# Kernel optimization log

Hardware: AMD Instinct MI355X
Metric: run time of the kernel (lower is better)

## Reference

```python
import jax, jax.numpy as jnp
import numpy as np

NU, NI = 100000, 50000      # global embedding table sizes
U, I = 50000, 20000         # nodes in this subgraph
E = 400000                  # edges per direction
HID, H = 512, 8
D = HID // H                # out_feats per head = 64
NEG_SLOPE = 0.2


def setup_inputs() -> dict:
    key = jax.random.key(0)
    ks = jax.random.split(key, 16)
    s = 1.0 / np.sqrt(HID)
    a = 1.0 / np.sqrt(D)
    return {
        'u_gid': jax.random.randint(ks[0], (U,), 0, NU),
        'i_gid': jax.random.randint(ks[1], (I,), 0, NI),
        'src_u': jax.random.randint(ks[2], (E,), 0, U),
        'dst_i': jax.random.randint(ks[3], (E,), 0, I),
        'user_emb': jax.random.normal(ks[4], (NU, HID), jnp.float32) * 0.02,
        'item_emb': jax.random.normal(ks[5], (NI, HID), jnp.float32) * 0.02,
        # 'interact' (user -> item) GATConv params
        'W_ui': jax.random.normal(ks[6], (HID, HID), jnp.float32) * s,
        'al_ui': jax.random.normal(ks[7], (H, D), jnp.float32) * a,
        'ar_ui': jax.random.normal(ks[8], (H, D), jnp.float32) * a,
        'b_ui': jnp.zeros((HID,), jnp.float32),
        # 'interact_rev' (item -> user) GATConv params
        'W_iu': jax.random.normal(ks[9], (HID, HID), jnp.float32) * s,
        'al_iu': jax.random.normal(ks[10], (H, D), jnp.float32) * a,
        'ar_iu': jax.random.normal(ks[11], (H, D), jnp.float32) * a,
        'b_iu': jnp.zeros((HID,), jnp.float32),
    }


def gat_conv(h_src, h_dst, src, dst, W, attn_l, attn_r, bias, n_dst):
    """DGL GATConv (eval mode, allow_zero_in_degree): [n_dst, H, D]."""
    fs = (h_src @ W).reshape(-1, H, D)            # [Ns,H,D]
    fd = (h_dst @ W).reshape(-1, H, D)            # [Nd,H,D]
    el = jnp.sum(fs * attn_l, axis=-1)            # [Ns,H]
    er = jnp.sum(fd * attn_r, axis=-1)            # [Nd,H]
    e = jax.nn.leaky_relu(el[src] + er[dst], NEG_SLOPE)   # [E,H]
    # segment softmax over incoming edges of each destination
    emax = jax.ops.segment_max(e, dst, num_segments=n_dst)[dst]
    ex = jnp.exp(e - emax)                        # [E,H]
    denom = jax.ops.segment_sum(ex, dst, num_segments=n_dst)[dst]
    alpha = ex / denom                            # [E,H]
    msg = fs[src] * alpha[:, :, None]             # [E,H,D]
    out = jax.ops.segment_sum(msg, dst, num_segments=n_dst)  # zero for isolated dst
    return out + bias.reshape(1, H, D)


def reference(u_gid, i_gid, src_u, dst_i, user_emb, item_emb,
              W_ui, al_ui, ar_ui, b_ui, W_iu, al_iu, ar_iu, b_iu):
    h_u0 = user_emb[u_gid]                        # [U,HID]
    h_i0 = item_emb[i_gid]                        # [I,HID]
    # 'interact': user -> item
    h_item = gat_conv(h_u0, h_i0, src_u, dst_i, W_ui, al_ui, ar_ui, b_ui, I)
    # 'interact_rev': item -> user (reversed edges)
    h_user = gat_conv(h_i0, h_u0, dst_i, src_u, W_iu, al_iu, ar_iu, b_iu, U)
    h_user = h_user.reshape(U, HID)
    h_item = h_item.reshape(I, HID)
    item_mean = jnp.mean(h_item, axis=0, keepdims=True)        # [1,HID]
    item_expand = jnp.broadcast_to(item_mean, (U, HID))
    return jnp.concatenate([h_user, item_expand], axis=1)      # [U, 2*HID]
```

## Files before the change

kernel.cpp:

```cpp
#include <hip/hip_runtime.h>
#include <hip/hip_bf16.h>
#include <stdint.h>

#define U_NODES 50000
#define I_NODES 20000
#define N_NODES 70000
#define M_PAD   70016
#define E_EDGES 400000
#define HID     512

typedef __attribute__((ext_vector_type(8))) short short8;
typedef __attribute__((ext_vector_type(4))) float floatx4;

static __device__ __forceinline__ uint16_t f2b(float f) {
    uint32_t x = __float_as_uint(f);
    x += 0x7fffu + ((x >> 16) & 1u);
    return (uint16_t)(x >> 16);
}
static __device__ __forceinline__ float b2f(short u) {
    return __uint_as_float(((uint32_t)(uint16_t)u) << 16);
}

__global__ void gather_cast(const int* __restrict__ u_gid, const int* __restrict__ i_gid,
                            const float* __restrict__ user_emb, const float* __restrict__ item_emb,
                            uint16_t* __restrict__ Xb)
{
    int t = blockIdx.x * 256 + threadIdx.x;
    int n = t >> 7;
    int j = (t & 127) << 2;
    uint2 o;
    if (n < N_NODES) {
        const float* src = (n < U_NODES) ? (user_emb + (size_t)u_gid[n] * HID)
                                         : (item_emb + (size_t)i_gid[n - U_NODES] * HID);
        float4 v = *(const float4*)(src + j);
        o.x = (uint32_t)f2b(v.x) | ((uint32_t)f2b(v.y) << 16);
        o.y = (uint32_t)f2b(v.z) | ((uint32_t)f2b(v.w) << 16);
    } else { o.x = 0u; o.y = 0u; }
    *(uint2*)(Xb + (size_t)n * HID + j) = o;
}

__global__ void prep_w(const float* __restrict__ Wui, const float* __restrict__ Wiu,
                       uint16_t* __restrict__ Wt)
{
    int t = blockIdx.x * 256 + threadIdx.x;
    int n = t >> 9, k = t & 511;
    float v = (n < 512) ? Wui[k * 512 + n] : Wiu[k * 512 + (n - 512)];
    Wt[(size_t)n * 512 + k] = f2b(v);
}

__global__ __launch_bounds__(256) void gemm_bf16(const uint16_t* __restrict__ Xb,
                                                 const uint16_t* __restrict__ Wt,
                                                 const float* __restrict__ al_ui, const float* __restrict__ ar_ui,
                                                 const float* __restrict__ al_iu, const float* __restrict__ ar_iu,
                                                 uint16_t* __restrict__ F,
                                                 float* __restrict__ ELui, float* __restrict__ ERui,
                                                 float* __restrict__ ELiu, float* __restrict__ ERiu)
{
    __shared__ __align__(16) uint16_t As[2][128 * 32];
    __shared__ __align__(16) uint16_t Bs[2][128 * 32];
    const int tid = threadIdx.x;
    const int wave = tid >> 6, lane = tid & 63;

    int bid = blockIdx.x;
    int x = bid & 7, ii = bid >> 3;
    int L = x * 547 + ii;
    const int m0 = (L >> 3) * 128;
    const int n0 = (L & 7) * 128;
    const int wm = (wave & 1) * 64;
    const int wn = (wave >> 1) * 64;

    const int rl2 = lane >> 2;
    const int sg = ((lane & 3) ^ ((lane >> 3) & 3)) * 8;
    const int ca = wave * 2, cb = wave * 2 + 1;
    const uint16_t* gA0 = Xb + (size_t)(m0 + ca * 16 + rl2) * HID + sg;
    const uint16_t* gA1 = Xb + (size_t)(m0 + cb * 16 + rl2) * HID + sg;
    const uint16_t* gB0 = Wt + (size_t)(n0 + ca * 16 + rl2) * HID + sg;
    const uint16_t* gB1 = Wt + (size_t)(n0 + cb * 16 + rl2) * HID + sg;

    floatx4 zero = {0.f, 0.f, 0.f, 0.f};
    floatx4 acc[4][4];
    #pragma unroll
    for (int a = 0; a < 4; ++a)
        #pragma unroll
        for (int b = 0; b < 4; ++b) acc[a][b] = zero;

    const int r = lane & 15, quad = lane >> 4;
    const int slq8 = (quad ^ ((r >> 1) & 3)) * 8;

#define STAGE(KO, BUF) do {                                                                         \
    __builtin_amdgcn_global_load_lds((const __attribute__((address_space(1))) void*)(gA0 + (KO)),   \
                                     (__attribute__((address_space(3))) void*)(&As[BUF][ca * 512]), 16, 0, 0); \
    __builtin_amdgcn_global_load_lds((const __attribute__((address_space(1))) void*)(gA1 + (KO)),   \
                                     (__attribute__((address_space(3))) void*)(&As[BUF][cb * 512]), 16, 0, 0); \
    __builtin_amdgcn_global_load_lds((const __attribute__((address_space(1))) void*)(gB0 + (KO)),   \
                                     (__attribute__((address_space(3))) void*)(&Bs[BUF][ca * 512]), 16, 0, 0); \
    __builtin_amdgcn_global_load_lds((const __attribute__((address_space(1))) void*)(gB1 + (KO)),   \
                                     (__attribute__((address_space(3))) void*)(&Bs[BUF][cb * 512]), 16, 0, 0); \
} while (0)

#define COMPUTE(BUF) do {                                                                           \
    short8 af[4], bf[4];                                                                            \
    _Pragma("unroll")                                                                               \
    for (int tm = 0; tm < 4; ++tm)                                                                  \
        af[tm] = *(const short8*)&As[BUF][(wm + tm * 16 + r) * 32 + slq8];                          \
    _Pragma("unroll")                                                                               \
    for (int tn = 0; tn < 4; ++tn)                                                                  \
        bf[tn] = *(const short8*)&Bs[BUF][(wn + tn * 16 + r) * 32 + slq8];                          \
    _Pragma("unroll")                                                                               \
    for (int tm = 0; tm < 4; ++tm)                                                                  \
        _Pragma("unroll")                                                                           \
        for (int tn = 0; tn < 4; ++tn)                                                              \
            acc[tm][tn] = __builtin_amdgcn_mfma_f32_16x16x32_bf16(af[tm], bf[tn], acc[tm][tn], 0, 0, 0); \
} while (0)

    STAGE(0, 0);
    __syncthreads();
    #pragma unroll
    for (int t = 0; t < 15; ++t) {
        const int bc = t & 1;
        STAGE((t + 1) * 32, bc ^ 1);
        COMPUTE(bc);
        __syncthreads();
    }
    COMPUTE(1);

#undef STAGE
#undef COMPUTE

    const bool collo = (n0 < 512);
    const bool allU = (m0 + 128 <= U_NODES);
    const bool allI = (m0 >= U_NODES);
    const bool storeb = (allU && collo) || (allI && !collo) || (!allU && !allI);

    const int colh = n0 + wn;
    const int h = (colh & 511) >> 6;
    const float* arv = collo ? ar_ui : ar_iu;
    float* ERp = collo ? ERui : ERiu;
    float ar4[4];
    #pragma unroll
    for (int tn = 0; tn < 4; ++tn) ar4[tn] = arv[h * 64 + tn * 16 + r];

    if (storeb) {
        const float* alv = collo ? al_ui : al_iu;
        float* ELp = collo ? ELui : ELiu;
        float al4[4];
        #pragma unroll
        for (int tn = 0; tn < 4; ++tn) al4[tn] = alv[h * 64 + tn * 16 + r];
        #pragma unroll
        for (int tm = 0; tm < 4; ++tm) {
            #pragma unroll
            for (int rr = 0; rr < 4; ++rr) {
                int row = m0 + wm + tm * 16 + quad * 4 + rr;
                float sl = 0.f, sr = 0.f;
                #pragma unroll
                for (int tn = 0; tn < 4; ++tn) {
                    sl += acc[tm][tn][rr] * al4[tn];
                    sr += acc[tm][tn][rr] * ar4[tn];
                }
                if (row < N_NODES && ((row < U_NODES) == collo)) {
                    #pragma unroll
                    for (int tn = 0; tn < 4; ++tn) {
                        int col = n0 + wn + tn * 16 + r;
                        F[(size_t)row * 1024 + col] = f2b(acc[tm][tn][rr]);
                    }
                }
                #pragma unroll
                for (int d = 1; d < 16; d <<= 1) {
                    sl += __shfl_xor(sl, d);
                    sr += __shfl_xor(sr, d);
                }
                if (r == 0 && row < N_NODES) {
                    ELp[row * 8 + h] = sl;
                    ERp[row * 8 + h] = sr;
                }
            }
        }
    } else {
        #pragma unroll
        for (int tm = 0; tm < 4; ++tm) {
            #pragma unroll
            for (int rr = 0; rr < 4; ++rr) {
                int row = m0 + wm + tm * 16 + quad * 4 + rr;
                float sr = 0.f;
                #pragma unroll
                for (int tn = 0; tn < 4; ++tn) sr += acc[tm][tn][rr] * ar4[tn];
                #pragma unroll
                for (int d = 1; d < 16; d <<= 1) sr += __shfl_xor(sr, d);
                if (r == 0 && row < N_NODES) ERp[row * 8 + h] = sr;
            }
        }
    }
}

__global__ void hist_kernel(const int* __restrict__ src_u, const int* __restrict__ dst_i,
                            int* __restrict__ counts_i, int* __restrict__ counts_u)
{
    int e = blockIdx.x * 256 + threadIdx.x;
    if (e >= E_EDGES) return;
    atomicAdd(&counts_i[dst_i[e]], 1);
    atomicAdd(&counts_u[src_u[e]], 1);
}

#define SCAN_CHUNK 1024
#define IBLKS ((I_NODES + SCAN_CHUNK - 1) / SCAN_CHUNK)
#define UBLKS ((U_NODES + SCAN_CHUNK - 1) / SCAN_CHUNK)

__global__ __launch_bounds__(256) void scan_level1(const int* __restrict__ counts_i,
                                                   const int* __restrict__ counts_u,
                                                   int* __restrict__ bsum)
{
    int b = blockIdx.x, t = threadIdx.x;
    const int* cnt; int n, base;
    if (b < IBLKS) { cnt = counts_i; n = I_NODES; base = b * SCAN_CHUNK; }
    else           { cnt = counts_u; n = U_NODES; base = (b - IBLKS) * SCAN_CHUNK; }
    int idx = base + t * 4;
    int s = 0;
    #pragma unroll
    for (int k = 0; k < 4; ++k) { int i = idx + k; if (i < n) s += cnt[i]; }
    __shared__ int ws[4];
    int lane = t & 63, w = t >> 6;
    int xv = s;
    #pragma unroll
    for (int d = 1; d < 64; d <<= 1) xv += __shfl_xor(xv, d);
    if (lane == 0) ws[w] = xv;
    __syncthreads();
    if (t == 0) bsum[b] = ws[0] + ws[1] + ws[2] + ws[3];
}

__global__ void scan_level2(const int* __restrict__ bsum, int* __restrict__ boff,
                            int* __restrict__ offs_i, int* __restrict__ offs_u)
{
    int t = threadIdx.x;
    int w = t >> 6, lane = t & 63;
    if (w == 0) {
        int v = (lane < IBLKS) ? bsum[lane] : 0;
        int xv = v;
        #pragma unroll
        for (int d = 1; d < 64; d <<= 1) { int y = __shfl_up(xv, d, 64); if (lane >= d) xv += y; }
        if (lane < IBLKS) boff[lane] = xv - v;
        if (lane == IBLKS - 1) offs_i[I_NODES] = xv;
    } else {
        int v = (lane < UBLKS) ? bsum[IBLKS + lane] : 0;
        int xv = v;
        #pragma unroll
        for (int d = 1; d < 64; d <<= 1) { int y = __shfl_up(xv, d, 64); if (lane >= d) xv += y; }
        if (lane < UBLKS) boff[IBLKS + lane] = xv - v;
        if (lane == UBLKS - 1) offs_u[U_NODES] = xv;
    }
}

__global__ __launch_bounds__(256) void scan_level3(const int* __restrict__ counts_i,
                                                   const int* __restrict__ counts_u,
                                                   const int* __restrict__ boff,
                                                   int* __restrict__ offs_i, int* __restrict__ cur_i,
                                                   int* __restrict__ offs_u, int* __restrict__ cur_u)
{
    int b = blockIdx.x, t = threadIdx.x;
    const int* cnt; int n, base; int* offs; int* cur;
    if (b < IBLKS) { cnt = counts_i; n = I_NODES; base = b * SCAN_CHUNK; offs = offs_i; cur = cur_i; }
    else           { cnt = counts_u; n = U_NODES; base = (b - IBLKS) * SCAN_CHUNK; offs = offs_u; cur = cur_u; }
    int idx = base + t * 4;
    int v[4]; int s = 0;
    #pragma unroll
    for (int k = 0; k < 4; ++k) { int i = idx + k; v[k] = (i < n) ? cnt[i] : 0; s += v[k]; }
    __shared__ int ws[4];
    int lane = t & 63, w = t >> 6;
    int xv = s;
    #pragma unroll
    for (int d = 1; d < 64; d <<= 1) { int y = __shfl_up(xv, d, 64); if (lane >= d) xv += y; }
    if (lane == 63) ws[w] = xv;
    __syncthreads();
    int wexcl = 0;
    #pragma unroll
    for (int k = 0; k < 4; ++k) if (k < w) wexcl += ws[k];
    int excl = boff[b] + wexcl + (xv - s);
    #pragma unroll
    for (int k = 0; k < 4; ++k) {
        int i = idx + k;
        if (i < n) { offs[i] = excl; cur[i] = excl; }
        excl += v[k];
    }
}

__global__ void scatter_kernel(const int* __restrict__ src_u, const int* __restrict__ dst_i,
                               int* __restrict__ cur_i, int* __restrict__ cur_u,
                               int* __restrict__ sorted_ui, int* __restrict__ sorted_iu)
{
    int e = blockIdx.x * 256 + threadIdx.x;
    if (e >= E_EDGES) return;
    int s = src_u[e], d = dst_i[e];
    int p = atomicAdd(&cur_i[d], 1);
    int q = atomicAdd(&cur_u[s], 1);
    sorted_ui[p] = s;
    sorted_iu[q] = U_NODES + d;
}

#define IBLK ((I_NODES + 3) / 4)
#define UBLK ((U_NODES + 3) / 4)
__global__ __launch_bounds__(256) void agg3_kernel(
    const int* __restrict__ offs_i, const int* __restrict__ sorted_ui,
    const int* __restrict__ offs_u, const int* __restrict__ sorted_iu,
    const float* __restrict__ ELui, const float* __restrict__ ERui,
    const float* __restrict__ ELiu, const float* __restrict__ ERiu,
    const uint16_t* __restrict__ F, const float* __restrict__ b_iu,
    float* __restrict__ out, float* __restrict__ itemF)
{
    int bid = blockIdx.x;
    int w = threadIdx.x >> 6, lane = threadIdx.x & 63;
    bool item_mode = bid < IBLK;
    const int* offs; const int* srcs; const float* el_tab; const float* er_tab;
    int dst, colbase, n_dst, dstnode;
    if (item_mode) {
        offs = offs_i; srcs = sorted_ui; el_tab = ELui; er_tab = ERui;
        dst = bid * 4 + w; colbase = 0; n_dst = I_NODES;
        dstnode = U_NODES + dst;
    } else {
        offs = offs_u; srcs = sorted_iu; el_tab = ELiu; er_tab = ERiu;
        dst = (bid - IBLK) * 4 + w; colbase = 512; n_dst = U_NODES;
        dstnode = dst;
    }
    if (dst >= n_dst) return;
    int h = lane >> 3;
    int j0 = offs[dst], j1 = offs[dst + 1];
    float er_h = er_tab[dstnode * 8 + h];

    float den = 0.f;
    float acc[8] = {0.f, 0.f, 0.f, 0.f, 0.f, 0.f, 0.f, 0.f};
    const int fb = colbase + lane * 8;
    int j = j0;
    for (; j + 8 <= j1; j += 8) {
        int s[8]; float wt[8]; short8 f[8];
        #pragma unroll
        for (int i = 0; i < 8; ++i) s[i] = srcs[j + i];
        #pragma unroll
        for (int i = 0; i < 8; ++i) {
            float e0 = el_tab[s[i] * 8 + h] + er_h;
            e0 = (e0 >= 0.f) ? e0 : 0.2f * e0;
            wt[i] = __expf(e0);
        }
        #pragma unroll
        for (int i = 0; i < 8; ++i) f[i] = *(const short8*)&F[(size_t)s[i] * 1024 + fb];
        #pragma unroll
        for (int i = 0; i < 8; ++i) {
            den += wt[i];
            #pragma unroll
            for (int q = 0; q < 8; ++q) acc[q] += wt[i] * b2f(f[i][q]);
        }
    }
    for (; j + 4 <= j1; j += 4) {
        int s[4]; float wt[4]; short8 f[4];
        #pragma unroll
        for (int i = 0; i < 4; ++i) s[i] = srcs[j + i];
        #pragma unroll
        for (int i = 0; i < 4; ++i) {
            float e0 = el_tab[s[i] * 8 + h] + er_h;
            e0 = (e0 >= 0.f) ? e0 : 0.2f * e0;
            wt[i] = __expf(e0);
        }
        #pragma unroll
        for (int i = 0; i < 4; ++i) f[i] = *(const short8*)&F[(size_t)s[i] * 1024 + fb];
        #pragma unroll
        for (int i = 0; i < 4; ++i) {
            den += wt[i];
            #pragma unroll
            for (int q = 0; q < 8; ++q) acc[q] += wt[i] * b2f(f[i][q]);
        }
    }
    for (; j < j1; ++j) {
        int s0 = srcs[j];
        float e0 = el_tab[s0 * 8 + h] + er_h;
        e0 = (e0 >= 0.f) ? e0 : 0.2f * e0;
        float w0 = __expf(e0);
        short8 f0 = *(const short8*)&F[(size_t)s0 * 1024 + fb];
        den += w0;
        #pragma unroll
        for (int q = 0; q < 8; ++q) acc[q] += w0 * b2f(f0[q]);
    }
    float inv = (j1 > j0) ? (1.f / den) : 0.f;
    #pragma unroll
    for (int q = 0; q < 8; ++q) acc[q] *= inv;

    int col = lane * 8;
    if (item_mode) {
        float* o = itemF + (size_t)dst * 512 + col;
        float4 v0 = {acc[0], acc[1], acc[2], acc[3]};
        float4 v1 = {acc[4], acc[5], acc[6], acc[7]};
        *(float4*)(o + 0) = v0;
        *(float4*)(o + 4) = v1;
    } else {
        float* o = out + (size_t)dst * 1024 + col;
        float4 v0 = {acc[0] + b_iu[col + 0], acc[1] + b_iu[col + 1],
                     acc[2] + b_iu[col + 2], acc[3] + b_iu[col + 3]};
        float4 v1 = {acc[4] + b_iu[col + 4], acc[5] + b_iu[col + 5],
                     acc[6] + b_iu[col + 6], acc[7] + b_iu[col + 7]};
        *(float4*)(o + 0) = v0;
        *(float4*)(o + 4) = v1;
    }
}

__global__ void item_reduce(const float* __restrict__ itemF, float* __restrict__ partial2)
{
    int b = blockIdx.x;
    int t = threadIdx.x;
    int cg = (t & 127) * 4;
    int rp = t >> 7;
    float4 s = {0.f, 0.f, 0.f, 0.f};
    int r0 = b * 125;
    for (int r = r0 + rp; r < r0 + 125; r += 2) {
        float4 v = *(const float4*)&itemF[(size_t)r * 512 + cg];
        s.x += v.x; s.y += v.y; s.z += v.z; s.w += v.w;
    }
    *(float4*)&partial2[(size_t)(b * 2 + rp) * 512 + cg] = s;
}

__global__ void meanvec_kernel(const float* __restrict__ partial2, const float* __restrict__ b_ui,
                               float* __restrict__ mean_vec)
{
    int c = threadIdx.x;
    float s = 0.f;
    for (int p = 0; p < 320; ++p) s += partial2[p * 512 + c];
    mean_vec[c] = s * (1.0f / (float)I_NODES) + b_ui[c];
}

__global__ void bcast_kernel(const float* __restrict__ mean_vec, float* __restrict__ out)
{
    int t = blockIdx.x * 256 + threadIdx.x;
    int u = t >> 7, q = t & 127;
    float4 v = ((const float4*)mean_vec)[q];
    *(float4*)(out + (size_t)u * 1024 + 512 + q * 4) = v;
}

extern "C" void kernel_launch(void* const* d_in, const int* in_sizes, int n_in,
                              void* d_out, int out_size, void* d_ws, size_t ws_size,
                              hipStream_t stream)
{
    const int*   u_gid    = (const int*)d_in[0];
    const int*   i_gid    = (const int*)d_in[1];
    const int*   src_u    = (const int*)d_in[2];
    const int*   dst_i    = (const int*)d_in[3];
    const float* user_emb = (const float*)d_in[4];
    const float* item_emb = (const float*)d_in[5];
    const float* W_ui     = (const float*)d_in[6];
    const float* al_ui    = (const float*)d_in[7];
    const float* ar_ui    = (const float*)d_in[8];
    const float* b_ui     = (const float*)d_in[9];
    const float* W_iu     = (const float*)d_in[10];
    const float* al_iu    = (const float*)d_in[11];
    const float* ar_iu    = (const float*)d_in[12];
    const float* b_iu     = (const float*)d_in[13];
    float* out = (float*)d_out;

    char* ws = (char*)d_ws;
    size_t off = 0;
    auto alloc = [&](size_t bytes) -> void* {
        void* p = ws + off;
        off = (off + bytes + 255) & ~(size_t)255;
        return p;
    };
    uint16_t* Xb   = (uint16_t*)alloc((size_t)M_PAD * 512 * 2);
    uint16_t* Wt   = (uint16_t*)alloc((size_t)1024 * 512 * 2);
    uint16_t* F    = (uint16_t*)alloc((size_t)M_PAD * 1024 * 2);
    float* ELui    = (float*)alloc((size_t)N_NODES * 8 * 4);
    float* ERui    = (float*)alloc((size_t)N_NODES * 8 * 4);
    float* ELiu    = (float*)alloc((size_t)N_NODES * 8 * 4);
    float* ERiu    = (float*)alloc((size_t)N_NODES * 8 * 4);
    int* offs_i    = (int*)alloc((size_t)(I_NODES + 1) * 4);
    int* cur_i     = (int*)alloc((size_t)I_NODES * 4);
    int* offs_u    = (int*)alloc((size_t)(U_NODES + 1) * 4);
    int* cur_u     = (int*)alloc((size_t)U_NODES * 4);
    int* sorted_ui = (int*)alloc((size_t)E_EDGES * 4);
    int* sorted_iu = (int*)alloc((size_t)E_EDGES * 4);
    int* bsum      = (int*)alloc((size_t)(IBLKS + UBLKS) * 4);
    int* boff      = (int*)alloc((size_t)(IBLKS + UBLKS) * 4);
    float* itemF   = (float*)alloc((size_t)I_NODES * 512 * 4);
    float* partial2= (float*)alloc((size_t)320 * 512 * 4);
    char* zptr = ws + off;
    int*   counts_i = (int*)alloc((size_t)I_NODES * 4);
    int*   counts_u = (int*)alloc((size_t)U_NODES * 4);
    size_t zbytes = (size_t)((ws + off) - zptr);
    float* mean_vec = (float*)alloc(512 * 4);
    (void)ws_size; (void)in_sizes; (void)n_in; (void)out_size;

    hipMemsetAsync(zptr, 0, zbytes, stream);
    prep_w<<<2048, 256, 0, stream>>>(W_ui, W_iu, Wt);
    gather_cast<<<M_PAD * 128 / 256, 256, 0, stream>>>(u_gid, i_gid, user_emb, item_emb, Xb);
    gemm_bf16<<<(M_PAD / 128) * 8, 256, 0, stream>>>(Xb, Wt, al_ui, ar_ui, al_iu, ar_iu,
                                                     F, ELui, ERui, ELiu, ERiu);
    hist_kernel<<<(E_EDGES + 255) / 256, 256, 0, stream>>>(src_u, dst_i, counts_i, counts_u);
    scan_level1<<<IBLKS + UBLKS, 256, 0, stream>>>(counts_i, counts_u, bsum);
    scan_level2<<<1, 128, 0, stream>>>(bsum, boff, offs_i, offs_u);
    scan_level3<<<IBLKS + UBLKS, 256, 0, stream>>>(counts_i, counts_u, boff,
                                                   offs_i, cur_i, offs_u, cur_u);
    scatter_kernel<<<(E_EDGES + 255) / 256, 256, 0, stream>>>(src_u, dst_i, cur_i, cur_u,
                                                              sorted_ui, sorted_iu);
    agg3_kernel<<<IBLK + UBLK, 256, 0, stream>>>(offs_i, sorted_ui, offs_u, sorted_iu,
                                                 ELui, ERui, ELiu, ERiu,
                                                 F, b_iu, out, itemF);
    item_reduce<<<160, 256, 0, stream>>>(itemF, partial2);
    meanvec_kernel<<<1, 512, 0, stream>>>(partial2, b_ui, mean_vec);
    bcast_kernel<<<U_NODES * 128 / 256, 256, 0, stream>>>(mean_vec, out);
}
```

Baseline: 775.9 us.

## Triple-buffer GEMM loads, fold scan level 2 into level 3, use nontemporal stores

The GEMM main loop moves from double to triple buffering in LDS. Loads run two stages ahead, with explicit vmcnt waits and a raw s_barrier, so more global-load latency is hidden behind MFMA work. The separate single-block scan_level2 launch is removed: each scan_level3 block reduces the preceding block sums itself, which drops one kernel launch and its serialization. Output stores in the aggregation and broadcast kernels become nontemporal to avoid polluting cache. The costs are more LDS per block, which may reduce occupancy, and some redundant bsum reduction work per scan block.

```diff
diff --git a/kernel.cpp b/kernel.cpp
--- a/kernel.cpp
+++ b/kernel.cpp
@@ -56,8 +56,8 @@
                                                  float* __restrict__ ELui, float* __restrict__ ERui,
                                                  float* __restrict__ ELiu, float* __restrict__ ERiu)
 {
-    __shared__ __align__(16) uint16_t As[2][128 * 32];
-    __shared__ __align__(16) uint16_t Bs[2][128 * 32];
+    __shared__ __align__(16) uint16_t As[3][128 * 32];
+    __shared__ __align__(16) uint16_t Bs[3][128 * 32];
     const int tid = threadIdx.x;
     const int wave = tid >> 6, lane = tid & 63;
 
@@ -114,15 +114,21 @@
 } while (0)
 
     STAGE(0, 0);
-    __syncthreads();
+    STAGE(32, 1);
     #pragma unroll
     for (int t = 0; t < 15; ++t) {
-        const int bc = t & 1;
-        STAGE((t + 1) * 32, bc ^ 1);
-        COMPUTE(bc);
-        __syncthreads();
-    }
-    COMPUTE(1);
+        asm volatile("s_waitcnt vmcnt(4)");
+        __builtin_amdgcn_sched_barrier(0);
+        __builtin_amdgcn_s_barrier();
+        __builtin_amdgcn_sched_barrier(0);
+        if (t < 14) STAGE((t + 2) * 32, (t + 2) % 3);
+        COMPUTE(t % 3);
+    }
+    asm volatile("s_waitcnt vmcnt(0)");
+    __builtin_amdgcn_sched_barrier(0);
+    __builtin_amdgcn_s_barrier();
+    __builtin_amdgcn_sched_barrier(0);
+    COMPUTE(0);
 
 #undef STAGE
 #undef COMPUTE
@@ -227,44 +233,32 @@
     if (t == 0) bsum[b] = ws[0] + ws[1] + ws[2] + ws[3];
 }
 
-__global__ void scan_level2(const int* __restrict__ bsum, int* __restrict__ boff,
-                            int* __restrict__ offs_i, int* __restrict__ offs_u)
-{
-    int t = threadIdx.x;
-    int w = t >> 6, lane = t & 63;
-    if (w == 0) {
-        int v = (lane < IBLKS) ? bsum[lane] : 0;
-        int xv = v;
-        #pragma unroll
-        for (int d = 1; d < 64; d <<= 1) { int y = __shfl_up(xv, d, 64); if (lane >= d) xv += y; }
-        if (lane < IBLKS) boff[lane] = xv - v;
-        if (lane == IBLKS - 1) offs_i[I_NODES] = xv;
-    } else {
-        int v = (lane < UBLKS) ? bsum[IBLKS + lane] : 0;
-        int xv = v;
-        #pragma unroll
-        for (int d = 1; d < 64; d <<= 1) { int y = __shfl_up(xv, d, 64); if (lane >= d) xv += y; }
-        if (lane < UBLKS) boff[IBLKS + lane] = xv - v;
-        if (lane == UBLKS - 1) offs_u[U_NODES] = xv;
-    }
-}
-
 __global__ __launch_bounds__(256) void scan_level3(const int* __restrict__ counts_i,
                                                    const int* __restrict__ counts_u,
-                                                   const int* __restrict__ boff,
+                                                   const int* __restrict__ bsum,
                                                    int* __restrict__ offs_i, int* __restrict__ cur_i,
                                                    int* __restrict__ offs_u, int* __restrict__ cur_u)
 {
     int b = blockIdx.x, t = threadIdx.x;
-    const int* cnt; int n, base; int* offs; int* cur;
-    if (b < IBLKS) { cnt = counts_i; n = I_NODES; base = b * SCAN_CHUNK; offs = offs_i; cur = cur_i; }
-    else           { cnt = counts_u; n = U_NODES; base = (b - IBLKS) * SCAN_CHUNK; offs = offs_u; cur = cur_u; }
+    const int* cnt; int n, base, segfirst, seglast; int* offs; int* cur;
+    if (b < IBLKS) { cnt = counts_i; n = I_NODES; base = b * SCAN_CHUNK; segfirst = 0; seglast = IBLKS - 1; offs = offs_i; cur = cur_i; }
+    else           { cnt = counts_u; n = U_NODES; base = (b - IBLKS) * SCAN_CHUNK; segfirst = IBLKS; seglast = IBLKS + UBLKS - 1; offs = offs_u; cur = cur_u; }
+    int lane = t & 63, w = t >> 6;
+
+    __shared__ int s_boff;
+    __shared__ int ws[4];
+    if (w == 0) {
+        int i = segfirst + lane;
+        int v = (i < b) ? bsum[i] : 0;
+        #pragma unroll
+        for (int d = 1; d < 64; d <<= 1) v += __shfl_xor(v, d);
+        if (lane == 0) s_boff = v;
+    }
+
     int idx = base + t * 4;
-    int v[4]; int s = 0;
-    #pragma unroll
-    for (int k = 0; k < 4; ++k) { int i = idx + k; v[k] = (i < n) ? cnt[i] : 0; s += v[k]; }
-    __shared__ int ws[4];
-    int lane = t & 63, w = t >> 6;
+    int v4[4]; int s = 0;
+    #pragma unroll
+    for (int k = 0; k < 4; ++k) { int i = idx + k; v4[k] = (i < n) ? cnt[i] : 0; s += v4[k]; }
     int xv = s;
     #pragma unroll
     for (int d = 1; d < 64; d <<= 1) { int y = __shfl_up(xv, d, 64); if (lane >= d) xv += y; }
@@ -273,13 +267,15 @@
     int wexcl = 0;
     #pragma unroll
     for (int k = 0; k < 4; ++k) if (k < w) wexcl += ws[k];
-    int excl = boff[b] + wexcl + (xv - s);
+    int excl = s_boff + wexcl + (xv - s);
     #pragma unroll
     for (int k = 0; k < 4; ++k) {
         int i = idx + k;
         if (i < n) { offs[i] = excl; cur[i] = excl; }
-        excl += v[k];
-    }
+        excl += v4[k];
+    }
+    if (t == 0 && b == seglast)
+        offs[n] = s_boff + ws[0] + ws[1] + ws[2] + ws[3];
 }
 
 __global__ void scatter_kernel(const int* __restrict__ src_u, const int* __restrict__ dst_i,
@@ -383,18 +379,18 @@
     int col = lane * 8;
     if (item_mode) {
         float* o = itemF + (size_t)dst * 512 + col;
-        float4 v0 = {acc[0], acc[1], acc[2], acc[3]};
-        float4 v1 = {acc[4], acc[5], acc[6], acc[7]};
-        *(float4*)(o + 0) = v0;
-        *(float4*)(o + 4) = v1;
+        floatx4 v0 = {acc[0], acc[1], acc[2], acc[3]};
+        floatx4 v1 = {acc[4], acc[5], acc[6], acc[7]};
+        __builtin_nontemporal_store(v0, (floatx4*)(o + 0));
+        __builtin_nontemporal_store(v1, (floatx4*)(o + 4));
     } else {
         float* o = out + (size_t)dst * 1024 + col;
-        float4 v0 = {acc[0] + b_iu[col + 0], acc[1] + b_iu[col + 1],
-                     acc[2] + b_iu[col + 2], acc[3] + b_iu[col + 3]};
-        float4 v1 = {acc[4] + b_iu[col + 4], acc[5] + b_iu[col + 5],
-                     acc[6] + b_iu[col + 6], acc[7] + b_iu[col + 7]};
-        *(float4*)(o + 0) = v0;
-        *(float4*)(o + 4) = v1;
+        floatx4 v0 = {acc[0] + b_iu[col + 0], acc[1] + b_iu[col + 1],
+                      acc[2] + b_iu[col + 2], acc[3] + b_iu[col + 3]};
+        floatx4 v1 = {acc[4] + b_iu[col + 4], acc[5] + b_iu[col + 5],
+                      acc[6] + b_iu[col + 6], acc[7] + b_iu[col + 7]};
+        __builtin_nontemporal_store(v0, (floatx4*)(o + 0));
+        __builtin_nontemporal_store(v1, (floatx4*)(o + 4));
     }
 }
 
@@ -426,8 +422,8 @@
 {
     int t = blockIdx.x * 256 + threadIdx.x;
     int u = t >> 7, q = t & 127;
-    float4 v = ((const float4*)mean_vec)[q];
-    *(float4*)(out + (size_t)u * 1024 + 512 + q * 4) = v;
+    floatx4 v = ((const floatx4*)mean_vec)[q];
+    __builtin_nontemporal_store(v, (floatx4*)(out + (size_t)u * 1024 + 512 + q * 4));
 }
 
 extern "C" void kernel_launch(void* const* d_in, const int* in_sizes, int n_in,
@@ -471,7 +467,6 @@
     int* sorted_ui = (int*)alloc((size_t)E_EDGES * 4);
     int* sorted_iu = (int*)alloc((size_t)E_EDGES * 4);
     int* bsum      = (int*)alloc((size_t)(IBLKS + UBLKS) * 4);
-    int* boff      = (int*)alloc((size_t)(IBLKS + UBLKS) * 4);
     float* itemF   = (float*)alloc((size_t)I_NODES * 512 * 4);
     float* partial2= (float*)alloc((size_t)320 * 512 * 4);
     char* zptr = ws + off;
@@ -488,8 +483,7 @@
                                                      F, ELui, ERui, ELiu, ERiu);
     hist_kernel<<<(E_EDGES + 255) / 256, 256, 0, stream>>>(src_u, dst_i, counts_i, counts_u);
     scan_level1<<<IBLKS + UBLKS, 256, 0, stream>>>(counts_i, counts_u, bsum);
-    scan_level2<<<1, 128, 0, stream>>>(bsum, boff, offs_i, offs_u);
-    scan_level3<<<IBLKS + UBLKS, 256, 0, stream>>>(counts_i, counts_u, boff,
+    scan_level3<<<IBLKS + UBLKS, 256, 0, stream>>>(counts_i, counts_u, bsum,
                                                    offs_i, cur_i, offs_u, cur_u);
     scatter_kernel<<<(E_EDGES + 255) / 256, 256, 0, stream>>>(src_u, dst_i, cur_i, cur_u,
                                                               sorted_ui, sorted_iu);
```

Result: faster. 756.9 us (-2.5%).
